# Performance work log

Measured on AMD Instinct MI355X. Metric: run time of the kernel, lower is better.

The kernel has to match this reference:

```python
import jax, jax.numpy as jnp
import numpy as np

N, T, C = 8, 2048, 1024   # batch, seq_len, n_embd (== num_cls)
NUM_CLS = 1024
LID, TL = 6, 12


def setup_inputs() -> dict:
    key = jax.random.key(0)
    ks = jax.random.split(key, 5)
    s = 1.0 / np.sqrt(C)
    x = jax.random.normal(ks[0], (N, T, C), jnp.float32)
    Wk = jax.random.normal(ks[1], (C, C), jnp.float32) * s
    Wv = jax.random.normal(ks[2], (C, C), jnp.float32) * s
    Wr = jax.random.normal(ks[3], (C, C), jnp.float32) * s
    Wo = jax.random.normal(ks[4], (NUM_CLS, C), jnp.float32) * s
    # faithful time-parameter initialization from __init__
    r0 = LID / (TL - 1)            # ratio_0_to_1
    r1 = 1.0 - LID / TL            # ratio_1_to_almost0
    ddd = (np.arange(C, dtype=np.float32) / C).reshape(1, 1, C)
    time_mix_k = jnp.asarray(ddd ** r1)
    time_mix_v = jnp.asarray(ddd ** r1 + 0.3 * r0)
    time_mix_r = jnp.asarray(ddd ** (0.5 * r1))
    time_decay = jnp.zeros((C,), jnp.float32)                 # decay_speed init
    time_first = jnp.full((C,), np.log(0.3), jnp.float32)
    last_x = jnp.zeros((N, 1, C), jnp.float32)                # init_x repeated
    state = jnp.zeros((N, 3, 1, C), jnp.float32)              # init_state repeated
    return {"x": x, "it": 0, "Wk": Wk, "Wv": Wv, "Wr": Wr, "Wo": Wo,
            "time_mix_k": time_mix_k, "time_mix_v": time_mix_v,
            "time_mix_r": time_mix_r, "time_decay": time_decay,
            "time_first": time_first, "last_x": last_x, "state": state}


def _wkv_with_eps(w, u, k, v, state):
    """Numerically-stabilized RWKV wkv scan. k,v: (N,T,C); state: (N,3,1,C)."""
    alpha = state[:, 0, -1]  # (N,C)
    beta = state[:, 1, -1]
    eps = state[:, 2, -1]

    def step(carry, kv):
        a, b, e = carry
        kt, vt = kv                      # each (N,C)
        ukt = u + kt
        tau = jnp.maximum(ukt, e)
        e1 = jnp.exp(e - tau)
        e2 = jnp.exp(ukt - tau)
        wkv_t = (e1 * a + e2 * vt) / (e1 * b + e2)
        w_eps = e - w
        e_n = jnp.maximum(w_eps, kt)
        e1n = jnp.exp(w_eps - e_n)
        e2n = jnp.exp(kt - e_n)
        return (e1n * a + e2n * vt, e1n * b + e2n, e_n), wkv_t

    kT = jnp.swapaxes(k, 0, 1)  # (T,N,C)
    vT = jnp.swapaxes(v, 0, 1)
    (alpha, beta, eps), wkv = jax.lax.scan(step, (alpha, beta, eps), (kT, vT))
    wkv = jnp.swapaxes(wkv, 0, 1)  # (N,T,C)
    last_state = jnp.stack([alpha, beta, eps], axis=1)[:, :, None, :]  # (N,3,1,C)
    return wkv, last_state


def reference(x, it, Wk, Wv, Wr, Wo, time_mix_k, time_mix_v, time_mix_r,
              time_decay, time_first, last_x, state):
    # time-mix blend (last_x = init_x zeros, broadcast over T as in the source)
    k = (x * time_mix_k + last_x * (1.0 - time_mix_k)) @ Wk.T
    v = (x * time_mix_v + last_x * (1.0 - time_mix_v)) @ Wv.T
    r = (x * time_mix_r + last_x * (1.0 - time_mix_r)) @ Wr.T
    sr = jax.nn.sigmoid(r)
    w = jnp.exp(time_decay)
    u = time_first
    wkv, _last_state = _wkv_with_eps(w, u, k, v, state)
    rwkv = (wkv * sr) @ Wo.T  # (N,T,NUM_CLS)
    return rwkv
```

## Files before the change

kernel.cpp:

```cpp
#include <hip/hip_runtime.h>
#include <hip/hip_bf16.h>
#include <stdint.h>


typedef float f4 __attribute__((ext_vector_type(4)));
typedef short bh8 __attribute__((ext_vector_type(8)));
typedef unsigned int u32;
typedef unsigned short u16;

__device__ __forceinline__ u32 cvt2bf(float a, float b) {
    __hip_bfloat162 h = __float22bfloat162_rn(make_float2(a, b));
    u32 u; __builtin_memcpy(&u, &h, 4); return u;
}
__device__ __forceinline__ float b2f(u16 u) {
    u32 x = (u32)u << 16; float f; __builtin_memcpy(&f, &x, 4); return f;
}
__device__ __forceinline__ u16 f2b(float f) {
    __hip_bfloat16 h = __float2bfloat16(f);
    u16 u; __builtin_memcpy(&u, &h, 2); return u;
}
__device__ __forceinline__ void gld_lds16(const void* g, void* l) {
    __builtin_amdgcn_global_load_lds(
        (const __attribute__((address_space(1))) u32*)g,
        (__attribute__((address_space(3))) u32*)l, 16, 0, 0);
}

__global__ __launch_bounds__(256, 2) void gemm_kvr(
    const u16* __restrict__ A, const u16* __restrict__ Wall, const float* __restrict__ bias,
    u16* __restrict__ Kb, u16* __restrict__ Vb, u16* __restrict__ SRb)
{
    __shared__ __align__(16) char pool[33792];
    u16* As = (u16*)pool;

    const int n0 = blockIdx.x * 128;
    const int m0 = blockIdx.y * 128;

    const int tid  = threadIdx.x;
    const int w    = tid >> 6;
    const int lane = tid & 63;

    const int srow = w * 32 + (lane >> 2);
    const int slot = lane & 3;
    const int chk  = slot ^ ((srow >> 1) & 3);
    const u16* gA0 = A + (size_t)(m0 + srow) * 1024 + chk * 8;
    const u16* gA1 = gA0 + (size_t)16 * 1024;
    const u16* gW0 = Wall + (size_t)(n0 + srow) * 1024 + chk * 8;
    const u16* gW1 = gW0 + (size_t)16 * 1024;
    u16* lA0 = As + (w * 32) * 32;
    u16* lA1 = lA0 + 16 * 32;

    const int fr   = lane & 15;
    const int quad = lane >> 4;
    const int wm = (w & 1) * 64;
    const int wn = (w >> 1) * 64;
    const int sp = quad ^ ((fr >> 1) & 3);
    const int aoff = (wm + fr) * 32 + sp * 8;
    const int boff = (wn + fr) * 32 + sp * 8;

    f4 acc[3][4][4];
#pragma unroll
    for (int p = 0; p < 3; p++)
#pragma unroll
        for (int i = 0; i < 4; i++)
#pragma unroll
            for (int j = 0; j < 4; j++) { f4 z = {0.f, 0.f, 0.f, 0.f}; acc[p][i][j] = z; }

    for (int kk = 0; kk < 1024; kk += 32) {
        gld_lds16(gA0 + kk, lA0);
        gld_lds16(gA1 + kk, lA1);
#pragma unroll
        for (int p = 0; p < 3; p++) {
            u16* lB0 = (u16*)(pool + 8192 + p * 8192) + (w * 32) * 32;
            gld_lds16(gW0 + (size_t)p * 1048576 + kk, lB0);
            gld_lds16(gW1 + (size_t)p * 1048576 + kk, lB0 + 16 * 32);
        }
        __syncthreads();
        bh8 af[4];
#pragma unroll
        for (int i = 0; i < 4; i++) af[i] = *(const bh8*)(As + aoff + i * 16 * 32);
#pragma unroll
        for (int p = 0; p < 3; p++) {
            const u16* Bs = (const u16*)(pool + 8192 + p * 8192);
            bh8 bf[4];
#pragma unroll
            for (int j = 0; j < 4; j++) bf[j] = *(const bh8*)(Bs + boff + j * 16 * 32);
#pragma unroll
            for (int i = 0; i < 4; i++)
#pragma unroll
                for (int j = 0; j < 4; j++)
                    acc[p][i][j] = __builtin_amdgcn_mfma_f32_16x16x32_bf16(af[i], bf[j], acc[p][i][j], 0, 0, 0);
        }
        __syncthreads();
    }

    const int rb = quad * 4;
    const int batch = m0 >> 11;
    u16* S = (u16*)pool;
    const int ch = lane & 15;
#pragma unroll
    for (int p = 0; p < 3; p++) {
        float bv[4];
#pragma unroll
        for (int j = 0; j < 4; j++) bv[j] = bias[p * 8192 + batch * 1024 + n0 + wn + j * 16 + fr];
        if (p) __syncthreads();
#pragma unroll
        for (int i = 0; i < 4; i++)
#pragma unroll
            for (int j = 0; j < 4; j++)
#pragma unroll
                for (int r = 0; r < 4; r++) {
                    float v = acc[p][i][j][r] + bv[j];
                    if (p == 2) v = __fdividef(1.0f, 1.0f + __expf(-v));
                    S[(wm + i * 16 + rb + r) * 132 + wn + j * 16 + fr] = f2b(v);
                }
        __syncthreads();
        u16* Y = p == 0 ? Kb : (p == 1 ? Vb : SRb);
#pragma unroll
        for (int t = 0; t < 8; t++) {
            int lrow = w * 32 + t * 4 + (lane >> 4);
            const u16* ptr = S + lrow * 132 + ch * 8;
            uint2 lo = *(const uint2*)ptr;
            uint2 hi = *(const uint2*)(ptr + 4);
            uint4 val = make_uint4(lo.x, lo.y, hi.x, hi.y);
            *(uint4*)(Y + (size_t)(m0 + lrow) * 1024 + n0 + ch * 8) = val;
        }
    }
}

__global__ __launch_bounds__(256, 4) void gemm_out(
    const u16* __restrict__ A, const u16* __restrict__ B, float* __restrict__ Y)
{
    __shared__ __align__(16) char pool[33792];
    u16* As = (u16*)pool;
    u16* Bs = (u16*)(pool + 8192);
    const int n0 = blockIdx.x * 128;
    const int m0 = blockIdx.y * 128;

    const int tid  = threadIdx.x;
    const int w    = tid >> 6;
    const int lane = tid & 63;
    const int srow = w * 32 + (lane >> 2);
    const int slot = lane & 3;
    const int chk  = slot ^ ((srow >> 1) & 3);
    const u16* gA0 = A + (size_t)(m0 + srow) * 1024 + chk * 8;
    const u16* gA1 = gA0 + (size_t)16 * 1024;
    const u16* gB0 = B + (size_t)(n0 + srow) * 1024 + chk * 8;
    const u16* gB1 = gB0 + (size_t)16 * 1024;
    u16* lA0 = As + (w * 32) * 32;
    u16* lA1 = lA0 + 16 * 32;
    u16* lB0 = Bs + (w * 32) * 32;
    u16* lB1 = lB0 + 16 * 32;

    const int fr   = lane & 15;
    const int quad = lane >> 4;
    const int wm = (w & 1) * 64;
    const int wn = (w >> 1) * 64;
    const int sp = quad ^ ((fr >> 1) & 3);
    const int aoff = (wm + fr) * 32 + sp * 8;
    const int boff = (wn + fr) * 32 + sp * 8;

    f4 acc[4][4];
#pragma unroll
    for (int i = 0; i < 4; i++)
#pragma unroll
        for (int j = 0; j < 4; j++) { f4 z = {0.f, 0.f, 0.f, 0.f}; acc[i][j] = z; }

    for (int kk = 0; kk < 1024; kk += 32) {
        gld_lds16(gA0 + kk, lA0);
        gld_lds16(gA1 + kk, lA1);
        gld_lds16(gB0 + kk, lB0);
        gld_lds16(gB1 + kk, lB1);
        __syncthreads();
        bh8 af[4], bf[4];
#pragma unroll
        for (int i = 0; i < 4; i++) af[i] = *(const bh8*)(As + aoff + i * 16 * 32);
#pragma unroll
        for (int j = 0; j < 4; j++) bf[j] = *(const bh8*)(Bs + boff + j * 16 * 32);
#pragma unroll
        for (int i = 0; i < 4; i++)
#pragma unroll
            for (int j = 0; j < 4; j++)
                acc[i][j] = __builtin_amdgcn_mfma_f32_16x16x32_bf16(af[i], bf[j], acc[i][j], 0, 0, 0);
        __syncthreads();
    }

    const int rb = quad * 4;
    float* Sf = (float*)pool;
#pragma unroll
    for (int i = 0; i < 4; i++) {
        __syncthreads();
#pragma unroll
        for (int j = 0; j < 4; j++)
#pragma unroll
            for (int r = 0; r < 4; r++) {
                int lrow = (w & 1) * 16 + rb + r;
                Sf[lrow * 132 + wn + j * 16 + fr] = acc[i][j][r];
            }
        __syncthreads();
#pragma unroll
        for (int t = 0; t < 4; t++) {
            int lrow = w * 8 + t * 2 + (lane >> 5);
            int ch = lane & 31;
            f4 val = *(const f4*)(Sf + lrow * 132 + ch * 4);
            int g = m0 + ((lrow >> 4) << 6) + i * 16 + (lrow & 15);
            *(f4*)(Y + (size_t)g * 1024 + n0 + ch * 4) = val;
        }
    }
}

__global__ __launch_bounds__(256) void prep_all(
    const float* __restrict__ x, const float* __restrict__ lastx,
    const float* __restrict__ Wk, const float* __restrict__ Wv,
    const float* __restrict__ Wr, const float* __restrict__ Wo,
    const float* __restrict__ tmk, const float* __restrict__ tmv, const float* __restrict__ tmr,
    u16* __restrict__ xb, u16* __restrict__ Wall, float* __restrict__ bias)
{
    int b = blockIdx.x;
    if (b < 16384) {
        int e = (b * 256 + threadIdx.x) << 2;
        f4 v = *(const f4*)(x + e);
        *(uint2*)(xb + e) = make_uint2(cvt2bf(v.x, v.y), cvt2bf(v.z, v.w));
    } else if (b < 20480) {
        int e = ((b - 16384) * 256 + threadIdx.x) << 2;
        int wid = e >> 20;
        int off = e & 1048575;
        int c = e & 1023;
        const float* src = wid == 0 ? Wk : (wid == 1 ? Wv : (wid == 2 ? Wr : Wo));
        f4 v = *(const f4*)(src + off);
        if (wid < 3) {
            const float* m = wid == 0 ? tmk : (wid == 1 ? tmv : tmr);
            v = v * *(const f4*)(m + c);
        }
        *(uint2*)(Wall + e) = make_uint2(cvt2bf(v.x, v.y), cvt2bf(v.z, v.w));
    } else {
        int wid = (b - 20480) * 4 + (threadIdx.x >> 6);
        int lane = threadIdx.x & 63;
        int proj = wid >> 10;
        int n = wid & 1023;
        const float* W = proj == 0 ? Wk : (proj == 1 ? Wv : Wr);
        const float* m = proj == 0 ? tmk : (proj == 1 ? tmv : tmr);
        float acc[8];
#pragma unroll
        for (int bb = 0; bb < 8; bb++) acc[bb] = 0.f;
        for (int c = lane; c < 1024; c += 64) {
            float wc = W[n * 1024 + c] * (1.0f - m[c]);
#pragma unroll
            for (int bb = 0; bb < 8; bb++) acc[bb] = fmaf(lastx[bb * 1024 + c], wc, acc[bb]);
        }
#pragma unroll
        for (int bb = 0; bb < 8; bb++) {
            float v = acc[bb];
#pragma unroll
            for (int sh = 32; sh >= 1; sh >>= 1) v += __shfl_xor(v, sh);
            if (lane == 0) bias[proj * 8192 + bb * 1024 + n] = v;
        }
    }
}

__global__ __launch_bounds__(256) void wkv_pass1(
    const u16* __restrict__ Kp, const u16* __restrict__ Vp,
    const float* __restrict__ tdec,
    float* __restrict__ Ca, float* __restrict__ Cb, float* __restrict__ Ce)
{
    int tid = blockIdx.x * 256 + threadIdx.x;
    int c = (tid & 511) << 1;
    int chunk = (tid >> 9) & 63;
    int n = tid >> 15;
    float w0 = __expf(tdec[c]), w1 = __expf(tdec[c + 1]);
    int base = (n * 2048 + chunk * 32) * 1024 + c;
    float a0 = 0.f, b0 = 0.f, e0 = -1e30f;
    float a1 = 0.f, b1 = 0.f, e1 = -1e30f;
#pragma unroll 4
    for (int i = 0; i < 32; i++) {
        u32 ku = *(const u32*)(Kp + base + (i << 10));
        u32 vu = *(const u32*)(Vp + base + (i << 10));
        float k0 = b2f((u16)ku), k1 = b2f((u16)(ku >> 16));
        float v0 = b2f((u16)vu), v1 = b2f((u16)(vu >> 16));
        float en0 = fmaxf(e0 - w0, k0);
        float f10 = __expf(e0 - w0 - en0), f20 = __expf(k0 - en0);
        a0 = fmaf(f10, a0, f20 * v0); b0 = fmaf(f10, b0, f20); e0 = en0;
        float en1 = fmaxf(e1 - w1, k1);
        float f11 = __expf(e1 - w1 - en1), f21 = __expf(k1 - en1);
        a1 = fmaf(f11, a1, f21 * v1); b1 = fmaf(f11, b1, f21); e1 = en1;
    }
    int oidx = ((n * 64 + chunk) << 10) + c;
    *(float2*)(Ca + oidx) = make_float2(a0, a1);
    *(float2*)(Cb + oidx) = make_float2(b0, b1);
    *(float2*)(Ce + oidx) = make_float2(e0, e1);
}

__global__ __launch_bounds__(256) void wkv_pass2(
    const float* __restrict__ state, const float* __restrict__ tdec,
    float* Ca, float* Cb, float* Ce)
{
    int tid = blockIdx.x * 256 + threadIdx.x;
    int c = tid & 1023;
    int n = tid >> 10;
    float a = state[(n * 3 + 0) * 1024 + c];
    float b = state[(n * 3 + 1) * 1024 + c];
    float e = state[(n * 3 + 2) * 1024 + c];
    float wL = __expf(tdec[c]) * 32.0f;
    for (int ch = 0; ch < 64; ++ch) {
        int idx = ((n * 64 + ch) << 10) + c;
        float ca = Ca[idx], cb = Cb[idx], ce = Ce[idx];
        Ca[idx] = a; Cb[idx] = b; Ce[idx] = e;
        float en = fmaxf(e - wL, ce);
        float f1 = __expf(e - wL - en);
        float f2 = __expf(ce - en);
        a = fmaf(f1, a, f2 * ca);
        b = fmaf(f1, b, f2 * cb);
        e = en;
    }
}

__global__ __launch_bounds__(256) void wkv_pass3(
    const u16* __restrict__ Kp, const u16* __restrict__ Vp, const u16* __restrict__ SRp,
    const float* __restrict__ Sa, const float* __restrict__ Sb, const float* __restrict__ Se,
    const float* __restrict__ tfirst, const float* __restrict__ tdec,
    u16* __restrict__ Pp)
{
    int tid = blockIdx.x * 256 + threadIdx.x;
    int c = (tid & 511) << 1;
    int chunk = (tid >> 9) & 63;
    int n = tid >> 15;
    int sidx = ((n * 64 + chunk) << 10) + c;
    float a0 = Sa[sidx], b0 = Sb[sidx], e0 = Se[sidx];
    float a1 = Sa[sidx + 1], b1 = Sb[sidx + 1], e1 = Se[sidx + 1];
    float u0 = tfirst[c], u1 = tfirst[c + 1];
    float w0 = __expf(tdec[c]), w1 = __expf(tdec[c + 1]);
    int base = (n * 2048 + chunk * 32) * 1024 + c;
#pragma unroll 2
    for (int i = 0; i < 32; i++) {
        u32 ku = *(const u32*)(Kp + base + (i << 10));
        u32 vu = *(const u32*)(Vp + base + (i << 10));
        u32 su = *(const u32*)(SRp + base + (i << 10));
        float k0 = b2f((u16)ku), k1 = b2f((u16)(ku >> 16));
        float v0 = b2f((u16)vu), v1 = b2f((u16)(vu >> 16));
        float s0 = b2f((u16)su), s1 = b2f((u16)(su >> 16));
        float t0 = fmaxf(u0 + k0, e0);
        float x10 = __expf(e0 - t0), x20 = __expf(u0 + k0 - t0);
        float wkv0 = __fdividef(fmaf(x10, a0, x20 * v0), fmaf(x10, b0, x20));
        float t1 = fmaxf(u1 + k1, e1);
        float x11 = __expf(e1 - t1), x21 = __expf(u1 + k1 - t1);
        float wkv1 = __fdividef(fmaf(x11, a1, x21 * v1), fmaf(x11, b1, x21));
        *(u32*)(Pp + base + (i << 10)) = (u32)f2b(wkv0 * s0) | ((u32)f2b(wkv1 * s1) << 16);
        float en0 = fmaxf(e0 - w0, k0);
        float f10 = __expf(e0 - w0 - en0), f20 = __expf(k0 - en0);
        a0 = fmaf(f10, a0, f20 * v0); b0 = fmaf(f10, b0, f20); e0 = en0;
        float en1 = fmaxf(e1 - w1, k1);
        float f11 = __expf(e1 - w1 - en1), f21 = __expf(k1 - en1);
        a1 = fmaf(f11, a1, f21 * v1); b1 = fmaf(f11, b1, f21); e1 = en1;
    }
}

extern "C" void kernel_launch(void* const* d_in, const int* in_sizes, int n_in,
                              void* d_out, int out_size, void* d_ws, size_t ws_size,
                              hipStream_t stream) {
    const float* x      = (const float*)d_in[0];
    const float* Wk     = (const float*)d_in[2];
    const float* Wv     = (const float*)d_in[3];
    const float* Wr     = (const float*)d_in[4];
    const float* Wo     = (const float*)d_in[5];
    const float* tmk    = (const float*)d_in[6];
    const float* tmv    = (const float*)d_in[7];
    const float* tmr    = (const float*)d_in[8];
    const float* tdec   = (const float*)d_in[9];
    const float* tfirst = (const float*)d_in[10];
    const float* lastx  = (const float*)d_in[11];
    const float* state  = (const float*)d_in[12];
    float* out = (float*)d_out;

    const size_t MB = 1024ull * 1024ull;
    char* ws = (char*)d_ws;
    u16* Kb   = (u16*)(ws);
    u16* Vb   = (u16*)(ws + 32 * MB);
    u16* SRb  = (u16*)(ws + 64 * MB);
    u16* xb   = (u16*)(ws + 96 * MB);
    u16* Wall = (u16*)(ws + 128 * MB);
    float* bias = (float*)(ws + 136 * MB);
    float* Ca = (float*)(ws + 137 * MB);
    float* Cb = (float*)(ws + 139 * MB);
    float* Ce = (float*)(ws + 141 * MB);
    u16* Pb = xb;

    dim3 blk(256);
    prep_all<<<21248, blk, 0, stream>>>(x, lastx, Wk, Wv, Wr, Wo, tmk, tmv, tmr, xb, Wall, bias);
    gemm_kvr<<<dim3(8, 128), blk, 0, stream>>>(xb, Wall, bias, Kb, Vb, SRb);
    wkv_pass1<<<1024, blk, 0, stream>>>(Kb, Vb, tdec, Ca, Cb, Ce);
    wkv_pass2<<<32, blk, 0, stream>>>(state, tdec, Ca, Cb, Ce);
    wkv_pass3<<<1024, blk, 0, stream>>>(Kb, Vb, SRb, Ca, Cb, Ce, tfirst, tdec, Pb);
    gemm_out<<<dim3(8, 128), blk, 0, stream>>>(Pb, Wall + 3145728, out);
}
```

Measured before the change: 366.2 us.

## Replace GEMMs with 256x256 double-buffered, phase-scheduled MFMA kernel

Replaces both the fused K/V/R GEMM and the output GEMM with one templated 256x256-tile kernel using 512 threads and 64-deep K steps. LDS is double-buffered, and global-to-LDS loads are interleaved between four MFMA phases with explicit waitcnt, barriers and setprio to overlap memory with compute. K/V/R now run as separate grid z-slices instead of three accumulators per block. The aim is higher data reuse and latency hiding in the GEMMs. In exchange it uses 128KB of LDS per block, many registers, and handwritten wait counts that must match the exact load order.

```diff
diff --git a/kernel.cpp b/kernel.cpp
--- a/kernel.cpp
+++ b/kernel.cpp
@@ -25,185 +25,177 @@
         (__attribute__((address_space(3))) u32*)l, 16, 0, 0);
 }
 
-__global__ __launch_bounds__(256, 2) void gemm_kvr(
-    const u16* __restrict__ A, const u16* __restrict__ Wall, const float* __restrict__ bias,
-    u16* __restrict__ Kb, u16* __restrict__ Vb, u16* __restrict__ SRb)
-{
-    __shared__ __align__(16) char pool[33792];
-    u16* As = (u16*)pool;
-
-    const int n0 = blockIdx.x * 128;
-    const int m0 = blockIdx.y * 128;
+
+#define BAR() __builtin_amdgcn_s_barrier()
+
+#define PH_MFMA(I0, J0) \
+  BAR(); \
+  asm volatile("s_waitcnt lgkmcnt(0)" ::: "memory"); \
+  __builtin_amdgcn_s_setprio(1); \
+  _Pragma("unroll") for (int ks = 0; ks < 2; ks++) \
+  _Pragma("unroll") for (int i = 0; i < 4; i++) \
+  _Pragma("unroll") for (int j = 0; j < 2; j++) \
+    acc[(I0)+i][(J0)+j] = __builtin_amdgcn_mfma_f32_16x16x32_bf16( \
+        af[i][ks], bf[j][ks], acc[(I0)+i][(J0)+j], 0, 0, 0); \
+  __builtin_amdgcn_s_setprio(0);
+
+#define GBODY(cA, cB, nA, nB, KKN, STG) do { \
+  const u16* ap0 = (cA) + (wm + fr) * 64 + cs0; \
+  const u16* ap1 = (cA) + (wm + fr) * 64 + (cs0 ^ 32); \
+  const u16* bp0 = (cB) + (wn + fr) * 64 + cs0; \
+  const u16* bp1 = (cB) + (wn + fr) * 64 + (cs0 ^ 32); \
+  bh8 af[4][2], bf[2][2]; \
+   \
+  _Pragma("unroll") for (int i = 0; i < 4; i++) { \
+    af[i][0] = *(const bh8*)(ap0 + i * 1024); af[i][1] = *(const bh8*)(ap1 + i * 1024); } \
+  _Pragma("unroll") for (int j = 0; j < 2; j++) { \
+    bf[j][0] = *(const bh8*)(bp0 + j * 1024); bf[j][1] = *(const bh8*)(bp1 + j * 1024); } \
+  if (STG) { \
+    gld_lds16(gB + srcB_lane + (KKN),                 (nB) + w * 1024); \
+    gld_lds16(gB + srcB_lane + 8192 + (KKN),          (nB) + w * 1024 + 512); \
+    gld_lds16(gB + srcB_lane + 131072 + (KKN),        (nB) + 8192 + w * 1024); \
+    gld_lds16(gB + srcB_lane + 131072 + 8192 + (KKN), (nB) + 8192 + w * 1024 + 512); } \
+  PH_MFMA(0, 0); \
+  BAR(); \
+   \
+  _Pragma("unroll") for (int j = 0; j < 2; j++) { \
+    bf[j][0] = *(const bh8*)(bp0 + (2 + j) * 1024); bf[j][1] = *(const bh8*)(bp1 + (2 + j) * 1024); } \
+  if (STG) { \
+    gld_lds16(gA + srcA_lane + (KKN),          (nA) + w * 512); \
+    gld_lds16(gA + srcA_lane + 131072 + (KKN), (nA) + 8192 + w * 512); } \
+  PH_MFMA(0, 2); \
+  if (STG) { asm volatile("s_waitcnt vmcnt(6)" ::: "memory"); } \
+  else     { asm volatile("s_waitcnt vmcnt(0)" ::: "memory"); } \
+  BAR(); \
+   \
+  _Pragma("unroll") for (int i = 0; i < 4; i++) { \
+    af[i][0] = *(const bh8*)(ap0 + (4 + i) * 1024); af[i][1] = *(const bh8*)(ap1 + (4 + i) * 1024); } \
+  _Pragma("unroll") for (int j = 0; j < 2; j++) { \
+    bf[j][0] = *(const bh8*)(bp0 + j * 1024); bf[j][1] = *(const bh8*)(bp1 + j * 1024); } \
+  if (STG) gld_lds16(gA + srcA_lane + 65536 + (KKN), (nA) + 4096 + w * 512); \
+  PH_MFMA(4, 0); \
+  BAR(); \
+   \
+  _Pragma("unroll") for (int j = 0; j < 2; j++) { \
+    bf[j][0] = *(const bh8*)(bp0 + (2 + j) * 1024); bf[j][1] = *(const bh8*)(bp1 + (2 + j) * 1024); } \
+  if (STG) gld_lds16(gA + srcA_lane + 131072 + 65536 + (KKN), (nA) + 12288 + w * 512); \
+  PH_MFMA(4, 2); \
+  if (STG) { asm volatile("s_waitcnt vmcnt(2)" ::: "memory"); } \
+  BAR(); \
+} while (0)
+
+template<int EPI>
+__global__ __launch_bounds__(512, 2) void gemm256(
+    const u16* __restrict__ Ag, const u16* __restrict__ Bg, const float* __restrict__ bias,
+    u16* __restrict__ Kb, u16* __restrict__ Vb, u16* __restrict__ SRb, float* __restrict__ Yf)
+{
+    __shared__ __align__(16) char pool[131072];
+    u16* A0s = (u16*)pool;
+    u16* B0s = A0s + 16384;
+    u16* A1s = B0s + 16384;
+    u16* B1s = A1s + 16384;
+
+    const int n0 = blockIdx.x * 256;
+    const int m0 = blockIdx.y * 256;
+    const int p  = (EPI == 0) ? blockIdx.z : 0;
+
+    const u16* gA = Ag + (size_t)m0 * 1024;
+    const u16* gB = Bg + (EPI == 0 ? (size_t)p * 1048576 : 0) + (size_t)n0 * 1024;
 
     const int tid  = threadIdx.x;
     const int w    = tid >> 6;
     const int lane = tid & 63;
-
-    const int srow = w * 32 + (lane >> 2);
-    const int slot = lane & 3;
-    const int chk  = slot ^ ((srow >> 1) & 3);
-    const u16* gA0 = A + (size_t)(m0 + srow) * 1024 + chk * 8;
-    const u16* gA1 = gA0 + (size_t)16 * 1024;
-    const u16* gW0 = Wall + (size_t)(n0 + srow) * 1024 + chk * 8;
-    const u16* gW1 = gW0 + (size_t)16 * 1024;
-    u16* lA0 = As + (w * 32) * 32;
-    u16* lA1 = lA0 + 16 * 32;
-
-    const int fr   = lane & 15;
-    const int quad = lane >> 4;
-    const int wm = (w & 1) * 64;
-    const int wn = (w >> 1) * 64;
-    const int sp = quad ^ ((fr >> 1) & 3);
-    const int aoff = (wm + fr) * 32 + sp * 8;
-    const int boff = (wn + fr) * 32 + sp * 8;
-
-    f4 acc[3][4][4];
-#pragma unroll
-    for (int p = 0; p < 3; p++)
-#pragma unroll
-        for (int i = 0; i < 4; i++)
-#pragma unroll
-            for (int j = 0; j < 4; j++) { f4 z = {0.f, 0.f, 0.f, 0.f}; acc[p][i][j] = z; }
-
-    for (int kk = 0; kk < 1024; kk += 32) {
-        gld_lds16(gA0 + kk, lA0);
-        gld_lds16(gA1 + kk, lA1);
-#pragma unroll
-        for (int p = 0; p < 3; p++) {
-            u16* lB0 = (u16*)(pool + 8192 + p * 8192) + (w * 32) * 32;
-            gld_lds16(gW0 + (size_t)p * 1048576 + kk, lB0);
-            gld_lds16(gW1 + (size_t)p * 1048576 + kk, lB0 + 16 * 32);
-        }
+    const int wr = w >> 2, wc = w & 3;
+    const int wm = wr * 128, wn = wc * 64;
+    const int fr = lane & 15, quad = lane >> 4;
+    const int cs0 = (quad ^ (fr & 7)) * 8;
+
+    const int l8 = lane >> 3, l7 = lane & 7;
+    const int chs = (l7 ^ l8) * 8;
+    const int srcA_lane = (w * 8 + l8) * 1024 + chs;
+    const int srcB_lane = (w * 16 + l8) * 1024 + chs;
+
+    f4 acc[8][4];
+#pragma unroll
+    for (int i = 0; i < 8; i++)
+#pragma unroll
+        for (int j = 0; j < 4; j++) { f4 z = {0.f, 0.f, 0.f, 0.f}; acc[i][j] = z; }
+
+#pragma unroll
+    for (int q = 0; q < 4; q++)
+        gld_lds16(gA + srcA_lane + q * 65536, A0s + q * 4096 + w * 512);
+#pragma unroll
+    for (int H = 0; H < 2; H++)
+#pragma unroll
+        for (int c = 0; c < 2; c++)
+            gld_lds16(gB + srcB_lane + H * 131072 + c * 8192, B0s + H * 8192 + w * 1024 + c * 512);
+    asm volatile("s_waitcnt vmcnt(0)" ::: "memory");
+    BAR();
+
+    for (int t = 0; t < 14; t += 2) {
+        GBODY(A0s, B0s, A1s, B1s, (t + 1) * 64, true);
+        GBODY(A1s, B1s, A0s, B0s, (t + 2) * 64, true);
+    }
+    GBODY(A0s, B0s, A1s, B1s, 15 * 64, true);
+    GBODY(A1s, B1s, A0s, B0s, 0, false);
+
+    if constexpr (EPI == 0) {
+        const int batch = m0 >> 11;
+        float bv[4];
+#pragma unroll
+        for (int j = 0; j < 4; j++) bv[j] = bias[p * 8192 + batch * 1024 + n0 + wn + j * 16 + fr];
         __syncthreads();
-        bh8 af[4];
-#pragma unroll
-        for (int i = 0; i < 4; i++) af[i] = *(const bh8*)(As + aoff + i * 16 * 32);
-#pragma unroll
-        for (int p = 0; p < 3; p++) {
-            const u16* Bs = (const u16*)(pool + 8192 + p * 8192);
-            bh8 bf[4];
-#pragma unroll
-            for (int j = 0; j < 4; j++) bf[j] = *(const bh8*)(Bs + boff + j * 16 * 32);
-#pragma unroll
-            for (int i = 0; i < 4; i++)
-#pragma unroll
-                for (int j = 0; j < 4; j++)
-                    acc[p][i][j] = __builtin_amdgcn_mfma_f32_16x16x32_bf16(af[i], bf[j], acc[p][i][j], 0, 0, 0);
-        }
-        __syncthreads();
-    }
-
-    const int rb = quad * 4;
-    const int batch = m0 >> 11;
-    u16* S = (u16*)pool;
-    const int ch = lane & 15;
-#pragma unroll
-    for (int p = 0; p < 3; p++) {
-        float bv[4];
-#pragma unroll
-        for (int j = 0; j < 4; j++) bv[j] = bias[p * 8192 + batch * 1024 + n0 + wn + j * 16 + fr];
-        if (p) __syncthreads();
-#pragma unroll
-        for (int i = 0; i < 4; i++)
+        u16* S = (u16*)pool;
+#pragma unroll
+        for (int i = 0; i < 8; i++)
 #pragma unroll
             for (int j = 0; j < 4; j++)
 #pragma unroll
                 for (int r = 0; r < 4; r++) {
-                    float v = acc[p][i][j][r] + bv[j];
+                    float v = acc[i][j][r] + bv[j];
                     if (p == 2) v = __fdividef(1.0f, 1.0f + __expf(-v));
-                    S[(wm + i * 16 + rb + r) * 132 + wn + j * 16 + fr] = f2b(v);
+                    int row = wm + i * 16 + quad * 4 + r;
+                    int col = wn + j * 16 + fr;
+                    int phys = (col >> 3) ^ (quad << 3);
+                    S[row * 256 + phys * 8 + (col & 7)] = f2b(v);
                 }
         __syncthreads();
         u16* Y = p == 0 ? Kb : (p == 1 ? Vb : SRb);
 #pragma unroll
-        for (int t = 0; t < 8; t++) {
-            int lrow = w * 32 + t * 4 + (lane >> 4);
-            const u16* ptr = S + lrow * 132 + ch * 8;
-            uint2 lo = *(const uint2*)ptr;
-            uint2 hi = *(const uint2*)(ptr + 4);
-            uint4 val = make_uint4(lo.x, lo.y, hi.x, hi.y);
-            *(uint4*)(Y + (size_t)(m0 + lrow) * 1024 + n0 + ch * 8) = val;
-        }
-    }
-}
-
-__global__ __launch_bounds__(256, 4) void gemm_out(
-    const u16* __restrict__ A, const u16* __restrict__ B, float* __restrict__ Y)
-{
-    __shared__ __align__(16) char pool[33792];
-    u16* As = (u16*)pool;
-    u16* Bs = (u16*)(pool + 8192);
-    const int n0 = blockIdx.x * 128;
-    const int m0 = blockIdx.y * 128;
-
-    const int tid  = threadIdx.x;
-    const int w    = tid >> 6;
-    const int lane = tid & 63;
-    const int srow = w * 32 + (lane >> 2);
-    const int slot = lane & 3;
-    const int chk  = slot ^ ((srow >> 1) & 3);
-    const u16* gA0 = A + (size_t)(m0 + srow) * 1024 + chk * 8;
-    const u16* gA1 = gA0 + (size_t)16 * 1024;
-    const u16* gB0 = B + (size_t)(n0 + srow) * 1024 + chk * 8;
-    const u16* gB1 = gB0 + (size_t)16 * 1024;
-    u16* lA0 = As + (w * 32) * 32;
-    u16* lA1 = lA0 + 16 * 32;
-    u16* lB0 = Bs + (w * 32) * 32;
-    u16* lB1 = lB0 + 16 * 32;
-
-    const int fr   = lane & 15;
-    const int quad = lane >> 4;
-    const int wm = (w & 1) * 64;
-    const int wn = (w >> 1) * 64;
-    const int sp = quad ^ ((fr >> 1) & 3);
-    const int aoff = (wm + fr) * 32 + sp * 8;
-    const int boff = (wn + fr) * 32 + sp * 8;
-
-    f4 acc[4][4];
-#pragma unroll
-    for (int i = 0; i < 4; i++)
-#pragma unroll
-        for (int j = 0; j < 4; j++) { f4 z = {0.f, 0.f, 0.f, 0.f}; acc[i][j] = z; }
-
-    for (int kk = 0; kk < 1024; kk += 32) {
-        gld_lds16(gA0 + kk, lA0);
-        gld_lds16(gA1 + kk, lA1);
-        gld_lds16(gB0 + kk, lB0);
-        gld_lds16(gB1 + kk, lB1);
-        __syncthreads();
-        bh8 af[4], bf[4];
-#pragma unroll
-        for (int i = 0; i < 4; i++) af[i] = *(const bh8*)(As + aoff + i * 16 * 32);
-#pragma unroll
-        for (int j = 0; j < 4; j++) bf[j] = *(const bh8*)(Bs + boff + j * 16 * 32);
-#pragma unroll
-        for (int i = 0; i < 4; i++)
-#pragma unroll
-            for (int j = 0; j < 4; j++)
-                acc[i][j] = __builtin_amdgcn_mfma_f32_16x16x32_bf16(af[i], bf[j], acc[i][j], 0, 0, 0);
-        __syncthreads();
-    }
-
-    const int rb = quad * 4;
-    float* Sf = (float*)pool;
-#pragma unroll
-    for (int i = 0; i < 4; i++) {
-        __syncthreads();
-#pragma unroll
-        for (int j = 0; j < 4; j++)
-#pragma unroll
-            for (int r = 0; r < 4; r++) {
-                int lrow = (w & 1) * 16 + rb + r;
-                Sf[lrow * 132 + wn + j * 16 + fr] = acc[i][j][r];
+        for (int rep = 0; rep < 16; rep++) {
+            int cid = rep * 512 + tid;
+            int row = cid >> 5, ch = cid & 31;
+            int phys = ch ^ (((row >> 2) & 3) << 3);
+            uint4 val = *(const uint4*)(S + row * 256 + phys * 8);
+            *(uint4*)(Y + (size_t)(m0 + row) * 1024 + n0 + ch * 8) = val;
+        }
+    } else {
+        float* Sf = (float*)pool;
+#pragma unroll
+        for (int h = 0; h < 2; h++) {
+            __syncthreads();
+            if (wr == h) {
+#pragma unroll
+                for (int i = 0; i < 8; i++)
+#pragma unroll
+                    for (int j = 0; j < 4; j++)
+#pragma unroll
+                        for (int r = 0; r < 4; r++) {
+                            int row = i * 16 + quad * 4 + r;
+                            int col = wn + j * 16 + fr;
+                            int phys = (col >> 2) ^ (quad << 4);
+                            Sf[row * 256 + phys * 4 + (col & 3)] = acc[i][j][r];
+                        }
             }
-        __syncthreads();
-#pragma unroll
-        for (int t = 0; t < 4; t++) {
-            int lrow = w * 8 + t * 2 + (lane >> 5);
-            int ch = lane & 31;
-            f4 val = *(const f4*)(Sf + lrow * 132 + ch * 4);
-            int g = m0 + ((lrow >> 4) << 6) + i * 16 + (lrow & 15);
-            *(f4*)(Y + (size_t)g * 1024 + n0 + ch * 4) = val;
+            __syncthreads();
+#pragma unroll
+            for (int rep = 0; rep < 16; rep++) {
+                int cid = rep * 512 + tid;
+                int row = cid >> 6, ch = cid & 63;
+                int phys = ch ^ (((row >> 2) & 3) << 4);
+                f4 val = *(const f4*)(Sf + row * 256 + phys * 4);
+                *(f4*)(Yf + (size_t)(m0 + h * 128 + row) * 1024 + n0 + ch * 4) = val;
+            }
         }
     }
 }
@@ -385,9 +377,10 @@
 
     dim3 blk(256);
     prep_all<<<21248, blk, 0, stream>>>(x, lastx, Wk, Wv, Wr, Wo, tmk, tmv, tmr, xb, Wall, bias);
-    gemm_kvr<<<dim3(8, 128), blk, 0, stream>>>(xb, Wall, bias, Kb, Vb, SRb);
+    gemm256<0><<<dim3(4, 64, 3), dim3(512), 0, stream>>>(xb, Wall, bias, Kb, Vb, SRb, nullptr);
     wkv_pass1<<<1024, blk, 0, stream>>>(Kb, Vb, tdec, Ca, Cb, Ce);
     wkv_pass2<<<32, blk, 0, stream>>>(state, tdec, Ca, Cb, Ce);
     wkv_pass3<<<1024, blk, 0, stream>>>(Kb, Vb, SRb, Ca, Cb, Ce, tfirst, tdec, Pb);
-    gemm_out<<<dim3(8, 128), blk, 0, stream>>>(Pb, Wall + 3145728, out);
-}
+    gemm256<1><<<dim3(4, 64, 1), dim3(512), 0, stream>>>(Pb, Wall + 3145728, nullptr,
+                                                         nullptr, nullptr, nullptr, out);
+}
```

Result: no change. 372.3 us (+1.7%).
